# Kernel tuning notes

Measured on AMD Instinct MI355X. Metric: run time of the kernel, lower is better.

The kernel has to match this reference:

```python
import jax, jax.numpy as jnp
import numpy as np

D_MODEL = 1024
NUM_HEADS = 16
DK = D_MODEL // NUM_HEADS
THETA = 10000.0
B, S = 4, 2048


def _rope(x, pos):
    # x: [B, H, S, dk], pos: [S] int positions
    half = DK // 2
    inv_freq = THETA ** (-jnp.arange(half, dtype=jnp.float32) * 2.0 / DK)  # [half]
    ang = pos.astype(jnp.float32)[:, None] * inv_freq[None, :]             # [S, half]
    cos, sin = jnp.cos(ang), jnp.sin(ang)                                  # [S, half]
    x_even = x[..., 0::2]
    x_odd = x[..., 1::2]
    out_even = x_even * cos - x_odd * sin
    out_odd = x_even * sin + x_odd * cos
    # interleave back to [..., dk]
    return jnp.stack([out_even, out_odd], axis=-1).reshape(x.shape)


def setup_inputs() -> dict:
    key = jax.random.key(0)
    ks = jax.random.split(key, 5)
    scale = 1.0 / np.sqrt(D_MODEL)
    return {
        "x": jax.random.normal(ks[0], (B, S, D_MODEL), dtype=jnp.float32),
        "token_position": jnp.arange(S, dtype=jnp.int32),
        "wq": jax.random.normal(ks[1], (D_MODEL, D_MODEL), dtype=jnp.float32) * scale,
        "wk": jax.random.normal(ks[2], (D_MODEL, D_MODEL), dtype=jnp.float32) * scale,
        "wv": jax.random.normal(ks[3], (D_MODEL, D_MODEL), dtype=jnp.float32) * scale,
        "wo": jax.random.normal(ks[4], (D_MODEL, D_MODEL), dtype=jnp.float32) * scale,
    }


def reference(x, token_position, wq, wk, wv, wo):
    b, s, _ = x.shape
    # QKV projections (torch Linear: y = x @ W.T), split heads -> [B, H, S, dk]
    def proj(w):
        y = jnp.einsum("bsd,ed->bse", x, w)
        return y.reshape(b, s, NUM_HEADS, DK).transpose(0, 2, 1, 3)
    q, k, v = proj(wq), proj(wk), proj(wv)
    q = _rope(q, token_position)
    k = _rope(k, token_position)
    # causal SDPA
    scores = jnp.einsum("bhqd,bhkd->bhqk", q, k) / jnp.sqrt(jnp.float32(DK))
    causal = jnp.tril(jnp.ones((s, s), dtype=bool))
    scores = jnp.where(causal, scores, -jnp.inf)
    attn = jax.nn.softmax(scores, axis=-1)
    out = jnp.einsum("bhqk,bhkd->bhqd", attn, v)          # [B, H, S, dv]
    out = out.transpose(0, 2, 1, 3).reshape(b, s, D_MODEL)  # merge heads
    return jnp.einsum("bsd,ed->bse", out, wo)             # output projection
```

## Files before the change

kernel.cpp:

```cpp
#include <hip/hip_runtime.h>


#define D_MODEL 1024
#define NH      16
#define DKH     64
#define SEQ     2048
#define BATCH   4
#define M_ROWS  (BATCH * SEQ)
#define SCALE_LOG2 0.180336875461f

typedef _Float16 f16;
typedef _Float16 f16x8 __attribute__((ext_vector_type(8)));
typedef _Float16 f16x4 __attribute__((ext_vector_type(4)));
typedef _Float16 f16x2 __attribute__((ext_vector_type(2)));
typedef __fp16   fp16x2n __attribute__((ext_vector_type(2)));
typedef float    f32x4 __attribute__((ext_vector_type(4)));
typedef unsigned short u16;
typedef unsigned int   u32;

__device__ __forceinline__ void glds16(const void* g, void* l) {
  __builtin_amdgcn_global_load_lds((const __attribute__((address_space(1))) void*)g,
                                   (__attribute__((address_space(3))) void*)l, 16, 0, 0);
}
__device__ __forceinline__ u32 pk(float a, float b) {
  union { fp16x2n h; u32 u; } c; c.h = __builtin_amdgcn_cvt_pkrtz(a, b); return c.u;
}

__global__ void cvt_f32_f16(const float* __restrict__ in, f16* __restrict__ out, int n) {
  int i = (blockIdx.x * blockDim.x + threadIdx.x) * 4;
  if (i >= n) return;
  float4 v = *(const float4*)(in + i);
  uint2 o; o.x = pk(v.x, v.y); o.y = pk(v.z, v.w);
  *(uint2*)(out + i) = o;
}

__global__ void cvt_w4(const float* __restrict__ w0, const float* __restrict__ w1,
                       const float* __restrict__ w2, const float* __restrict__ w3,
                       f16* __restrict__ o0, f16* __restrict__ o1,
                       f16* __restrict__ o2, f16* __restrict__ o3, int n) {
  const float* src; f16* dst;
  switch (blockIdx.y) {
    case 0:  src = w0; dst = o0; break;
    case 1:  src = w1; dst = o1; break;
    case 2:  src = w2; dst = o2; break;
    default: src = w3; dst = o3; break;
  }
  int i = (blockIdx.x * blockDim.x + threadIdx.x) * 4;
  if (i >= n) return;
  float4 v = *(const float4*)(src + i);
  uint2 o; o.x = pk(v.x, v.y); o.y = pk(v.z, v.w);
  *(uint2*)(dst + i) = o;
}

template<int MODE>
__global__ __launch_bounds__(256) void gemm_glds(const f16* __restrict__ A,
                                                 const f16* __restrict__ W,
                                                 void* __restrict__ C0,
                                                 void* __restrict__ C1,
                                                 void* __restrict__ C2,
                                                 int K) {
  __shared__ f16 As[128][64];
  __shared__ f16 Bs[128][64];
  const int tid  = threadIdx.x;
  const int m0   = blockIdx.y * 128;
  const int n0   = blockIdx.x * 128;
  const int wave = tid >> 6, lane = tid & 63;
  const int quad = lane >> 4, l16 = lane & 15;
  const int wm = (wave >> 1) * 64, wn = (wave & 1) * 64;

  f32x4 acc[4][4];
#pragma unroll
  for (int i = 0; i < 4; ++i)
#pragma unroll
    for (int j = 0; j < 4; ++j) acc[i][j] = (f32x4){0.f, 0.f, 0.f, 0.f};

  for (int k0 = 0; k0 < K; k0 += 64) {
    if (k0) __syncthreads();
#pragma unroll
    for (int i = 0; i < 4; ++i) {
      int ci  = i * 256 + tid;
      int row = ci >> 3, ch = ci & 7;
      glds16(A + (size_t)(m0 + row) * K + k0 + ch * 8,
             (char*)&As[0][0] + (size_t)(i * 256 + (tid & 192)) * 16);
      glds16(W + (size_t)(n0 + row) * K + k0 + ch * 8,
             (char*)&Bs[0][0] + (size_t)(i * 256 + (tid & 192)) * 16);
    }
    __syncthreads();
#pragma unroll
    for (int kk = 0; kk < 64; kk += 32) {
      f16x8 af[4], bfr[4];
#pragma unroll
      for (int mi = 0; mi < 4; ++mi)
        af[mi] = *(const f16x8*)&As[wm + mi * 16 + l16][kk + quad * 8];
#pragma unroll
      for (int ni = 0; ni < 4; ++ni)
        bfr[ni] = *(const f16x8*)&Bs[wn + ni * 16 + l16][kk + quad * 8];
#pragma unroll
      for (int mi = 0; mi < 4; ++mi)
#pragma unroll
        for (int ni = 0; ni < 4; ++ni)
          acc[mi][ni] = __builtin_amdgcn_mfma_f32_16x16x32_f16(af[mi], bfr[ni], acc[mi][ni], 0, 0, 0);
    }
  }

  if (MODE == 1) {
    f16* dst; int nb;
    if (n0 < 1024)      { dst = (f16*)C0; nb = n0; }
    else if (n0 < 2048) { dst = (f16*)C1; nb = n0 - 1024; }
    else                { dst = (f16*)C2; nb = n0 - 2048; }
#pragma unroll
    for (int mi = 0; mi < 4; ++mi)
#pragma unroll
      for (int ni = 0; ni < 4; ++ni)
#pragma unroll
        for (int r = 0; r < 4; ++r) {
          int row = m0 + wm + mi * 16 + quad * 4 + r;
          int col = nb + wn + ni * 16 + l16;
          dst[(size_t)row * 1024 + col] = (f16)acc[mi][ni][r];
        }
  } else {
    float* dst = (float*)C0;
#pragma unroll
    for (int mi = 0; mi < 4; ++mi)
#pragma unroll
      for (int ni = 0; ni < 4; ++ni)
#pragma unroll
        for (int r = 0; r < 4; ++r) {
          int row = m0 + wm + mi * 16 + quad * 4 + r;
          int col = n0 + wn + ni * 16 + l16;
          dst[(size_t)row * 1024 + col] = acc[mi][ni][r];
        }
  }
}

__global__ void rope_kernel(f16* __restrict__ Q, f16* __restrict__ Kb,
                            const int* __restrict__ pos, int npairs) {
  int p = blockIdx.x * blockDim.x + threadIdx.x;
  if (p >= npairs) return;
  int i = p & 31;
  int s = (p >> 9) & (SEQ - 1);
  float inv = __builtin_amdgcn_exp2f(-0.41524101186092029f * (float)i);
  float ang = (float)pos[s] * inv;
  float c = cosf(ang), sn = sinf(ang);

  union { u32 u; f16x2 h; } uq, uk;
  uq.u = *(u32*)(Q + 2 * (size_t)p);
  float qe = (float)uq.h[0], qo = (float)uq.h[1];
  *(u32*)(Q + 2 * (size_t)p) = pk(qe * c - qo * sn, qe * sn + qo * c);

  uk.u = *(u32*)(Kb + 2 * (size_t)p);
  float ke = (float)uk.h[0], ko = (float)uk.h[1];
  *(u32*)(Kb + 2 * (size_t)p) = pk(ke * c - ko * sn, ke * sn + ko * c);
}

__global__ __launch_bounds__(256, 3) void flash_attn(const f16* __restrict__ Q,
                                                     const f16* __restrict__ Kg,
                                                     const f16* __restrict__ Vg,
                                                     f16* __restrict__ O) {
  __shared__ char smem[34560];
  f16*  KsL        = (f16*)smem;
  u32   (*Vt)[67]  = (u32(*)[67])(smem + 16384);
  float (*Red)[66] = (float(*)[66])smem;
  float (*Lbuf)[4] = (float(*)[4])(smem + 33536);

  const int tid  = threadIdx.x;
  const int bh   = blockIdx.x;
  const int b    = bh >> 4, h = bh & 15;
  const int qblk = 31 - (int)blockIdx.y;
  const int q0   = qblk * 64;
  const int wave = tid >> 6, lane = tid & 63;
  const int quad = lane >> 4, l16 = lane & 15;
  const int nkt  = (qblk + 2) >> 1;

  f16x8 qf[4][2];
#pragma unroll
  for (int nt = 0; nt < 4; ++nt)
#pragma unroll
    for (int ks = 0; ks < 2; ++ks) {
      f16x8 qv = *(const f16x8*)(Q + ((size_t)(b * SEQ + q0 + nt * 16 + l16)) * D_MODEL
                                   + h * DKH + ks * 32 + quad * 8);
      qf[nt][ks] = qv * (f16)SCALE_LOG2;
    }

  f32x4 o[4][4];
#pragma unroll
  for (int md = 0; md < 4; ++md)
#pragma unroll
    for (int nt = 0; nt < 4; ++nt) o[md][nt] = (f32x4){0.f, 0.f, 0.f, 0.f};
  float lacc[4] = {0.f, 0.f, 0.f, 0.f};

  const int kp = tid >> 3, dc = (tid & 7) * 8;

  for (int t = 0; t < nkt; ++t) {
    const int kt = t * 128;
    const f16* vb = Vg + ((size_t)(b * SEQ + kt + 2 * kp)) * D_MODEL + h * DKH + dc;
    uint4 v0 = *(const uint4*)vb;
    uint4 v1 = *(const uint4*)(vb + D_MODEL);
    uint4 v2 = *(const uint4*)(vb + 64 * D_MODEL);
    uint4 v3 = *(const uint4*)(vb + 65 * D_MODEL);

    if (t) __syncthreads();
#pragma unroll
    for (int i = 0; i < 4; ++i) {
      int ci = i * 256 + tid;
      int row = ci >> 3, gc = (ci & 7) ^ (row & 7);
      glds16(Kg + ((size_t)(b * SEQ + kt + row)) * D_MODEL + h * DKH + gc * 8,
             smem + (size_t)(i * 256 + (tid & 192)) * 16);
    }
    {
      union { uint4 u; u16 s[8]; } a0, a1, a2, a3;
      a0.u = v0; a1.u = v1; a2.u = v2; a3.u = v3;
#pragma unroll
      for (int j = 0; j < 8; ++j) {
        Vt[dc + j][kp]      = (u32)a0.s[j] | ((u32)a1.s[j] << 16);
        Vt[dc + j][32 + kp] = (u32)a2.s[j] | ((u32)a3.s[j] << 16);
      }
    }
    __syncthreads();

    f16x4 pb[2][4];
#pragma unroll
    for (int mt = 0; mt < 2; ++mt) {
      const int krow = wave * 32 + mt * 16 + l16;
      const int s0 = quad ^ (krow & 7);
      f16x8 ka0 = *(const f16x8*)(KsL + krow * 64 + s0 * 8);
      f16x8 ka1 = *(const f16x8*)(KsL + krow * 64 + (s0 ^ 4) * 8);
      const int keyb = kt + wave * 32 + mt * 16 + quad * 4;
#pragma unroll
      for (int nt = 0; nt < 4; ++nt) {
        f32x4 c = (f32x4){0.f, 0.f, 0.f, 0.f};
        c = __builtin_amdgcn_mfma_f32_16x16x32_f16(ka0, qf[nt][0], c, 0, 0, 0);
        c = __builtin_amdgcn_mfma_f32_16x16x32_f16(ka1, qf[nt][1], c, 0, 0, 0);
        const int q = q0 + nt * 16 + l16;
        float p0 = __builtin_amdgcn_exp2f(c[0]);
        float p1 = __builtin_amdgcn_exp2f(c[1]);
        float p2 = __builtin_amdgcn_exp2f(c[2]);
        float p3 = __builtin_amdgcn_exp2f(c[3]);
        if (t == nkt - 1) {
          p0 = (keyb + 0 <= q) ? p0 : 0.f;
          p1 = (keyb + 1 <= q) ? p1 : 0.f;
          p2 = (keyb + 2 <= q) ? p2 : 0.f;
          p3 = (keyb + 3 <= q) ? p3 : 0.f;
        }
        lacc[nt] += (p0 + p1) + (p2 + p3);
        union { u32 w[2]; f16x4 v; } pp;
        pp.w[0] = pk(p0, p1); pp.w[1] = pk(p2, p3);
        pb[mt][nt] = pp.v;
      }
    }

#pragma unroll
    for (int md = 0; md < 4; ++md)
#pragma unroll
      for (int ks2 = 0; ks2 < 2; ++ks2) {
        const u32* vp = &Vt[md * 16 + l16][wave * 16 + ks2 * 8 + quad * 2];
        union { u32 x[2]; f16x4 v; } va;
        va.x[0] = vp[0]; va.x[1] = vp[1];
#pragma unroll
        for (int nt = 0; nt < 4; ++nt)
          o[md][nt] = __builtin_amdgcn_mfma_f32_16x16x16f16(va.v, pb[ks2][nt], o[md][nt], 0, 0, 0);
      }
  }

  __syncthreads();
  for (int w = 0; w < 4; ++w) {
    if (wave == w) {
#pragma unroll
      for (int md = 0; md < 4; ++md)
#pragma unroll
        for (int nt = 0; nt < 4; ++nt)
#pragma unroll
          for (int r = 0; r < 4; ++r) {
            float* s = &Red[md * 16 + quad * 4 + r][nt * 16 + l16];
            if (w == 0) *s = o[md][nt][r]; else *s += o[md][nt][r];
          }
#pragma unroll
      for (int nt = 0; nt < 4; ++nt) {
        float* ls = &Lbuf[nt * 16 + l16][quad];
        if (w == 0) *ls = lacc[nt]; else *ls += lacc[nt];
      }
    }
    __syncthreads();
  }

  {
    const int q = tid & 63, dc4 = (tid >> 6) * 16;
    float lsum = Lbuf[q][0] + Lbuf[q][1] + Lbuf[q][2] + Lbuf[q][3];
    float linv = __builtin_amdgcn_rcpf(lsum);
    union { uint4 u[2]; u32 w[8]; } ov;
#pragma unroll
    for (int i = 0; i < 8; ++i)
      ov.w[i] = pk(Red[dc4 + 2 * i][q] * linv, Red[dc4 + 2 * i + 1][q] * linv);
    f16* op = O + ((size_t)(b * SEQ + q0 + q)) * D_MODEL + h * DKH + dc4;
    *(uint4*)op = ov.u[0];
    *(uint4*)(op + 8) = ov.u[1];
  }
}

extern "C" void kernel_launch(void* const* d_in, const int* in_sizes, int n_in,
                              void* d_out, int out_size, void* d_ws, size_t ws_size,
                              hipStream_t stream) {
  const float* x      = (const float*)d_in[0];
  const int*   tokpos = (const int*)d_in[1];
  const float* wq     = (const float*)d_in[2];
  const float* wk     = (const float*)d_in[3];
  const float* wv     = (const float*)d_in[4];
  const float* wo     = (const float*)d_in[5];
  float* out = (float*)d_out;

  char* ws = (char*)d_ws;
  f16* Xb  = (f16*)(ws + 0);
  f16* Wqb = (f16*)(ws + 16777216);
  f16* Wkb = (f16*)(ws + 18874368);
  f16* Wvb = (f16*)(ws + 20971520);
  f16* Wob = (f16*)(ws + 23068672);
  f16* Qb  = (f16*)(ws + 25165824);
  f16* Kb  = (f16*)(ws + 41943040);
  f16* Vb  = (f16*)(ws + 58720256);
  f16* Ob  = Xb;

  const int nX = BATCH * SEQ * D_MODEL;
  const int nW = D_MODEL * D_MODEL;

  cvt_f32_f16<<<nX / 1024, 256, 0, stream>>>(x, Xb, nX);
  cvt_w4<<<dim3(nW / 1024, 4), 256, 0, stream>>>(wq, wk, wv, wo, Wqb, Wkb, Wvb, Wob, nW);

  gemm_glds<1><<<dim3(24, 64), 256, 0, stream>>>(Xb, Wqb, Qb, Kb, Vb, D_MODEL);

  rope_kernel<<<(BATCH * SEQ * (D_MODEL / 2)) / 256, 256, 0, stream>>>(
      Qb, Kb, tokpos, BATCH * SEQ * (D_MODEL / 2));

  flash_attn<<<dim3(BATCH * NH, 32), 256, 0, stream>>>(Qb, Kb, Vb, Ob);

  gemm_glds<0><<<dim3(8, 64), 256, 0, stream>>>(Ob, Wob, out, nullptr, nullptr, D_MODEL);
}
```

Baseline: 269.3 us.

## Fuse RoPE into QKV GEMM epilogue, merge conversions, parallelize attention reduction

Applies rotary embedding inside the QKV projection epilogue on fp32 accumulators. Adjacent lanes are paired with a lane shuffle, which removes the separate RoPE kernel and its extra read/write pass over Q and K. The input and weight fp32-to-fp16 conversions are merged into one launch. The flash-attention cross-wave output reduction uses two buffers and fewer barriers instead of four serialized wave passes. The GEMM epilogue now does extra trig work per element and flash attention uses slightly more shared memory.

```diff
diff --git a/kernel.cpp b/kernel.cpp
--- a/kernel.cpp
+++ b/kernel.cpp
@@ -8,6 +8,7 @@
 #define BATCH   4
 #define M_ROWS  (BATCH * SEQ)
 #define SCALE_LOG2 0.180336875461f
+#define ROPE_L2    0.41524101186092029f
 
 typedef _Float16 f16;
 typedef _Float16 f16x8 __attribute__((ext_vector_type(8)));
@@ -26,27 +27,20 @@
   union { fp16x2n h; u32 u; } c; c.h = __builtin_amdgcn_cvt_pkrtz(a, b); return c.u;
 }
 
-__global__ void cvt_f32_f16(const float* __restrict__ in, f16* __restrict__ out, int n) {
-  int i = (blockIdx.x * blockDim.x + threadIdx.x) * 4;
-  if (i >= n) return;
-  float4 v = *(const float4*)(in + i);
-  uint2 o; o.x = pk(v.x, v.y); o.y = pk(v.z, v.w);
-  *(uint2*)(out + i) = o;
-}
-
-__global__ void cvt_w4(const float* __restrict__ w0, const float* __restrict__ w1,
-                       const float* __restrict__ w2, const float* __restrict__ w3,
-                       f16* __restrict__ o0, f16* __restrict__ o1,
-                       f16* __restrict__ o2, f16* __restrict__ o3, int n) {
-  const float* src; f16* dst;
-  switch (blockIdx.y) {
-    case 0:  src = w0; dst = o0; break;
-    case 1:  src = w1; dst = o1; break;
-    case 2:  src = w2; dst = o2; break;
-    default: src = w3; dst = o3; break;
-  }
-  int i = (blockIdx.x * blockDim.x + threadIdx.x) * 4;
-  if (i >= n) return;
+__global__ void cvt_all(const float* __restrict__ x,
+                        const float* __restrict__ w0, const float* __restrict__ w1,
+                        const float* __restrict__ w2, const float* __restrict__ w3,
+                        f16* __restrict__ xo, f16* __restrict__ o0, f16* __restrict__ o1,
+                        f16* __restrict__ o2, f16* __restrict__ o3) {
+  int blk = blockIdx.x;
+  const float* src; f16* dst; int off;
+  if (blk < 8192) { src = x; dst = xo; off = blk; }
+  else {
+    int t = blk - 8192; int w = t >> 10; off = t & 1023;
+    switch (w) { case 0: src = w0; dst = o0; break;  case 1: src = w1; dst = o1; break;
+                 case 2: src = w2; dst = o2; break;  default: src = w3; dst = o3; break; }
+  }
+  int i = (off * 256 + threadIdx.x) * 4;
   float4 v = *(const float4*)(src + i);
   uint2 o; o.x = pk(v.x, v.y); o.y = pk(v.z, v.w);
   *(uint2*)(dst + i) = o;
@@ -58,6 +52,7 @@
                                                  void* __restrict__ C0,
                                                  void* __restrict__ C1,
                                                  void* __restrict__ C2,
+                                                 const int* __restrict__ pos,
                                                  int K) {
   __shared__ f16 As[128][64];
   __shared__ f16 Bs[128][64];
@@ -108,16 +103,43 @@
     if (n0 < 1024)      { dst = (f16*)C0; nb = n0; }
     else if (n0 < 2048) { dst = (f16*)C1; nb = n0 - 1024; }
     else                { dst = (f16*)C2; nb = n0 - 2048; }
-#pragma unroll
-    for (int mi = 0; mi < 4; ++mi)
-#pragma unroll
-      for (int ni = 0; ni < 4; ++ni)
+    if (n0 < 2048) {
+      float invf[4], sgn[4];
+#pragma unroll
+      for (int ni = 0; ni < 4; ++ni) {
+        int dk = (wn + ni * 16 + l16) & 63;
+        invf[ni] = __builtin_amdgcn_exp2f(-ROPE_L2 * (float)(dk >> 1));
+        sgn[ni]  = (dk & 1) ? 1.f : -1.f;
+      }
+#pragma unroll
+      for (int mi = 0; mi < 4; ++mi)
 #pragma unroll
         for (int r = 0; r < 4; ++r) {
           int row = m0 + wm + mi * 16 + quad * 4 + r;
-          int col = nb + wn + ni * 16 + l16;
-          dst[(size_t)row * 1024 + col] = (f16)acc[mi][ni][r];
+          float ps = (float)pos[row & (SEQ - 1)];
+#pragma unroll
+          for (int ni = 0; ni < 4; ++ni) {
+            float ang = ps * invf[ni];
+            float c = __cosf(ang), sn = __sinf(ang);
+            float v = acc[mi][ni][r];
+            float p = __shfl_xor(v, 1);
+            float ov = fmaf(p * sgn[ni], sn, v * c);
+            int col = nb + wn + ni * 16 + l16;
+            dst[(size_t)row * 1024 + col] = (f16)ov;
+          }
         }
+    } else {
+#pragma unroll
+      for (int mi = 0; mi < 4; ++mi)
+#pragma unroll
+        for (int ni = 0; ni < 4; ++ni)
+#pragma unroll
+          for (int r = 0; r < 4; ++r) {
+            int row = m0 + wm + mi * 16 + quad * 4 + r;
+            int col = nb + wn + ni * 16 + l16;
+            dst[(size_t)row * 1024 + col] = (f16)acc[mi][ni][r];
+          }
+    }
   } else {
     float* dst = (float*)C0;
 #pragma unroll
@@ -133,35 +155,16 @@
   }
 }
 
-__global__ void rope_kernel(f16* __restrict__ Q, f16* __restrict__ Kb,
-                            const int* __restrict__ pos, int npairs) {
-  int p = blockIdx.x * blockDim.x + threadIdx.x;
-  if (p >= npairs) return;
-  int i = p & 31;
-  int s = (p >> 9) & (SEQ - 1);
-  float inv = __builtin_amdgcn_exp2f(-0.41524101186092029f * (float)i);
-  float ang = (float)pos[s] * inv;
-  float c = cosf(ang), sn = sinf(ang);
-
-  union { u32 u; f16x2 h; } uq, uk;
-  uq.u = *(u32*)(Q + 2 * (size_t)p);
-  float qe = (float)uq.h[0], qo = (float)uq.h[1];
-  *(u32*)(Q + 2 * (size_t)p) = pk(qe * c - qo * sn, qe * sn + qo * c);
-
-  uk.u = *(u32*)(Kb + 2 * (size_t)p);
-  float ke = (float)uk.h[0], ko = (float)uk.h[1];
-  *(u32*)(Kb + 2 * (size_t)p) = pk(ke * c - ko * sn, ke * sn + ko * c);
-}
-
 __global__ __launch_bounds__(256, 3) void flash_attn(const f16* __restrict__ Q,
                                                      const f16* __restrict__ Kg,
                                                      const f16* __restrict__ Vg,
                                                      f16* __restrict__ O) {
-  __shared__ char smem[34560];
-  f16*  KsL        = (f16*)smem;
-  u32   (*Vt)[67]  = (u32(*)[67])(smem + 16384);
-  float (*Red)[66] = (float(*)[66])smem;
-  float (*Lbuf)[4] = (float(*)[4])(smem + 33536);
+  __shared__ char smem[38400];
+  f16*  KsL         = (f16*)smem;
+  u32   (*Vt)[67]   = (u32(*)[67])(smem + 16384);
+  float (*Red0)[66] = (float(*)[66])smem;
+  float (*Red1)[66] = (float(*)[66])(smem + 16896);
+  float (*Lb)[17]   = (float(*)[17])(smem + 33792);
 
   const int tid  = threadIdx.x;
   const int bh   = blockIdx.x;
@@ -263,34 +266,46 @@
   }
 
   __syncthreads();
-  for (int w = 0; w < 4; ++w) {
-    if (wave == w) {
+  {
+    float (*Rw)[66] = (wave >= 2) ? Red1 : Red0;
+    if ((wave & 1) == 0) {
 #pragma unroll
       for (int md = 0; md < 4; ++md)
 #pragma unroll
         for (int nt = 0; nt < 4; ++nt)
 #pragma unroll
-          for (int r = 0; r < 4; ++r) {
-            float* s = &Red[md * 16 + quad * 4 + r][nt * 16 + l16];
-            if (w == 0) *s = o[md][nt][r]; else *s += o[md][nt][r];
-          }
-#pragma unroll
-      for (int nt = 0; nt < 4; ++nt) {
-        float* ls = &Lbuf[nt * 16 + l16][quad];
-        if (w == 0) *ls = lacc[nt]; else *ls += lacc[nt];
-      }
+          for (int r = 0; r < 4; ++r)
+            Rw[md * 16 + quad * 4 + r][nt * 16 + l16] = o[md][nt][r];
+    }
+#pragma unroll
+    for (int nt = 0; nt < 4; ++nt)
+      Lb[nt * 16 + l16][wave * 4 + quad] = lacc[nt];
+    __syncthreads();
+    if (wave & 1) {
+#pragma unroll
+      for (int md = 0; md < 4; ++md)
+#pragma unroll
+        for (int nt = 0; nt < 4; ++nt)
+#pragma unroll
+          for (int r = 0; r < 4; ++r)
+            Rw[md * 16 + quad * 4 + r][nt * 16 + l16] += o[md][nt][r];
     }
     __syncthreads();
   }
 
   {
     const int q = tid & 63, dc4 = (tid >> 6) * 16;
-    float lsum = Lbuf[q][0] + Lbuf[q][1] + Lbuf[q][2] + Lbuf[q][3];
+    float lsum = 0.f;
+#pragma unroll
+    for (int j = 0; j < 16; ++j) lsum += Lb[q][j];
     float linv = __builtin_amdgcn_rcpf(lsum);
     union { uint4 u[2]; u32 w[8]; } ov;
 #pragma unroll
-    for (int i = 0; i < 8; ++i)
-      ov.w[i] = pk(Red[dc4 + 2 * i][q] * linv, Red[dc4 + 2 * i + 1][q] * linv);
+    for (int i = 0; i < 8; ++i) {
+      float f0 = Red0[dc4 + 2 * i][q]     + Red1[dc4 + 2 * i][q];
+      float f1 = Red0[dc4 + 2 * i + 1][q] + Red1[dc4 + 2 * i + 1][q];
+      ov.w[i] = pk(f0 * linv, f1 * linv);
+    }
     f16* op = O + ((size_t)(b * SEQ + q0 + q)) * D_MODEL + h * DKH + dc4;
     *(uint4*)op = ov.u[0];
     *(uint4*)(op + 8) = ov.u[1];
@@ -319,18 +334,11 @@
   f16* Vb  = (f16*)(ws + 58720256);
   f16* Ob  = Xb;
 
-  const int nX = BATCH * SEQ * D_MODEL;
-  const int nW = D_MODEL * D_MODEL;
-
-  cvt_f32_f16<<<nX / 1024, 256, 0, stream>>>(x, Xb, nX);
-  cvt_w4<<<dim3(nW / 1024, 4), 256, 0, stream>>>(wq, wk, wv, wo, Wqb, Wkb, Wvb, Wob, nW);
-
-  gemm_glds<1><<<dim3(24, 64), 256, 0, stream>>>(Xb, Wqb, Qb, Kb, Vb, D_MODEL);
-
-  rope_kernel<<<(BATCH * SEQ * (D_MODEL / 2)) / 256, 256, 0, stream>>>(
-      Qb, Kb, tokpos, BATCH * SEQ * (D_MODEL / 2));
+  cvt_all<<<12288, 256, 0, stream>>>(x, wq, wk, wv, wo, Xb, Wqb, Wkb, Wvb, Wob);
+
+  gemm_glds<1><<<dim3(24, 64), 256, 0, stream>>>(Xb, Wqb, Qb, Kb, Vb, tokpos, D_MODEL);
 
   flash_attn<<<dim3(BATCH * NH, 32), 256, 0, stream>>>(Qb, Kb, Vb, Ob);
 
-  gemm_glds<0><<<dim3(8, 64), 256, 0, stream>>>(Ob, Wob, out, nullptr, nullptr, D_MODEL);
-}
+  gemm_glds<0><<<dim3(8, 64), 256, 0, stream>>>(Ob, Wob, out, nullptr, nullptr, nullptr, D_MODEL);
+}
```

Result: faster. 255.1 us (-5.3%).
